# Performance work log

Hardware: AMD Instinct MI355X
Metric: run time of the kernel (lower is better)

Reference implementation:

```python
import jax, jax.numpy as jnp
import numpy as np

B, L, E = 4, 2048, 1024
H, D = 16, 64  # heads, head_dim; H*D == E


def setup_inputs() -> dict:
    key = jax.random.key(0)
    ks = jax.random.split(key, 6)
    s = 0.02
    return {
        "x": jax.random.normal(ks[0], (B, L, E), dtype=jnp.float32),
        "Wq": jax.random.normal(ks[1], (E, H * D), dtype=jnp.float32) * s,
        "Wk": jax.random.normal(ks[2], (E, H * D), dtype=jnp.float32) * s,
        "Wv": jax.random.normal(ks[3], (E, H * D), dtype=jnp.float32) * s,
        "Wo": jax.random.normal(ks[4], (H * D, E), dtype=jnp.float32) * s,
        "bo": jax.random.normal(ks[5], (E,), dtype=jnp.float32) * s,
    }


def reference(x, Wq, Wk, Wv, Wo, bo):
    b, l, e = x.shape
    q = (x @ Wq).reshape(b, l, H, D)
    k = (x @ Wk).reshape(b, l, H, D)
    v = (x @ Wv).reshape(b, l, H, D)
    # NOTE: original scales by sqrt(embed_size), not sqrt(head_dim)
    energy = jnp.einsum('nqhd,nkhd->nhqk', q, k)
    attn = jax.nn.softmax(energy / jnp.sqrt(jnp.float32(e)), axis=3)
    out = jnp.einsum('nhql,nlhd->nqhd', attn, v).reshape(b, l, H * D)
    return out @ Wo + bo
```

## Files before the change

### kernel.cpp

```cpp
#include <hip/hip_runtime.h>

#define B_ 4
#define L_ 2048
#define E_ 1024
#define H_ 16
#define D_ 64
#define CSCALE 0.045084960222629414f

typedef short s16x8 __attribute__((ext_vector_type(8)));
typedef short s16x4 __attribute__((ext_vector_type(4)));
typedef float f32x4 __attribute__((ext_vector_type(4)));

__device__ __forceinline__ unsigned short f2bf(float f) {
  union { float f; unsigned int u; } v;
  v.f = f;
  unsigned int u = v.u;
  u += 0x7fffu + ((u >> 16) & 1u);
  return (unsigned short)(u >> 16);
}

__device__ __forceinline__ unsigned short f2bf_pos(float f) {
  union { float f; unsigned int u; } v;
  v.f = f;
  return (unsigned short)((v.u + 0x8000u) >> 16);
}

__device__ __forceinline__ void async16(const void* g, void* l) {
  __builtin_amdgcn_global_load_lds(
      (__attribute__((address_space(1))) void*)(g),
      (__attribute__((address_space(3))) void*)(l), 16, 0, 0);
}

__global__ void k_prep(const float* __restrict__ x,
                       const float* __restrict__ Wq, const float* __restrict__ Wk,
                       const float* __restrict__ Wv, const float* __restrict__ Wo,
                       unsigned short* __restrict__ xb,
                       unsigned short* __restrict__ Wt, unsigned short* __restrict__ WoT) {
  __shared__ float t[32][33];
  int bid = blockIdx.x, tid = threadIdx.x;
  if (bid < 8192) {
    int i = bid * 256 + tid;
    float4 v = ((const float4*)x)[i];
    ushort4 o;
    o.x = f2bf(v.x); o.y = f2bf(v.y); o.z = f2bf(v.z); o.w = f2bf(v.w);
    ((ushort4*)xb)[i] = o;
    return;
  }
  int tt = bid - 8192;
  int wsel = tt >> 10, tile = tt & 1023;
  const float* in = (wsel == 0) ? Wq : (wsel == 1) ? Wk : (wsel == 2) ? Wv : Wo;
  unsigned short* out = (wsel == 0) ? Wt : (wsel == 1) ? Wt + (1u << 20)
                        : (wsel == 2) ? Wt + (2u << 20) : WoT;
  int bx = tile & 31, by = tile >> 5;
  int tx = tid & 31, ty = tid >> 5;
  int xcol = bx * 32 + tx;
  int y0 = by * 32;
#pragma unroll
  for (int i = 0; i < 4; ++i)
    t[ty + i * 8][tx] = in[(size_t)(y0 + ty + i * 8) * 1024 + xcol];
  __syncthreads();
  int xo = by * 32 + tx;
  int yo0 = bx * 32;
#pragma unroll
  for (int i = 0; i < 4; ++i)
    out[(size_t)(yo0 + ty + i * 8) * 1024 + xo] = f2bf(t[tx][ty + i * 8]);
}

__global__ __launch_bounds__(256) void k_gemm_qkvt(
    const unsigned short* __restrict__ xb, const unsigned short* __restrict__ Wt,
    unsigned short* __restrict__ Qb, unsigned short* __restrict__ Kb,
    unsigned short* __restrict__ Vt) {
  __shared__ __align__(16) unsigned short As[128 * 32];
  __shared__ __align__(16) unsigned short Bs[128 * 32];
  const int bid = blockIdx.x;
  const int tid = threadIdx.x;
  const int w = tid >> 6, lane = tid & 63;
  const int quad = lane >> 4, mrow = lane & 15;
  const bool isQK = bid < 1024;
  int m0, n0;
  const unsigned short *PA, *PB;
  if (isQK) {
    m0 = (bid & 63) * 128;
    n0 = (bid >> 6) * 128;
    PA = xb + (size_t)m0 * 1024;
    PB = Wt + (size_t)n0 * 1024;
  } else {
    int g = bid - 1024;
    m0 = (g & 7) * 128;
    n0 = (g >> 3) * 128;
    PA = Wt + (2u << 20) + (size_t)m0 * 1024;
    PB = xb + (size_t)n0 * 1024;
  }
  const int wr = (w >> 1) * 64, wc = (w & 1) * 64;
  const f32x4 fz = {0.f, 0.f, 0.f, 0.f};
  f32x4 acc[4][4];
#pragma unroll
  for (int a = 0; a < 4; ++a)
#pragma unroll
    for (int b = 0; b < 4; ++b) acc[a][b] = fz;

  for (int kt = 0; kt < 32; ++kt) {
    __syncthreads();
#pragma unroll
    for (int r = 0; r < 2; ++r) {
      int c = r * 256 + tid;
      int row = c >> 2, cc = c & 3;
      async16(PA + (size_t)row * 1024 + kt * 32 + cc * 8, &As[c * 8]);
    }
#pragma unroll
    for (int r = 0; r < 2; ++r) {
      int c = r * 256 + tid;
      int row = c >> 2, cc = c & 3;
      async16(PB + (size_t)row * 1024 + kt * 32 + cc * 8, &Bs[c * 8]);
    }
    __syncthreads();
    s16x8 a[4], b[4];
#pragma unroll
    for (int mt = 0; mt < 4; ++mt)
      a[mt] = *(const s16x8*)&As[(wr + mt * 16 + mrow) * 32 + quad * 8];
#pragma unroll
    for (int nt = 0; nt < 4; ++nt)
      b[nt] = *(const s16x8*)&Bs[(wc + nt * 16 + mrow) * 32 + quad * 8];
#pragma unroll
    for (int mt = 0; mt < 4; ++mt)
#pragma unroll
      for (int nt = 0; nt < 4; ++nt)
        acc[mt][nt] = __builtin_amdgcn_mfma_f32_16x16x32_bf16(a[mt], b[nt], acc[mt][nt], 0, 0, 0);
  }
  if (isQK) {
#pragma unroll
    for (int mt = 0; mt < 4; ++mt)
#pragma unroll
      for (int nt = 0; nt < 4; ++nt)
#pragma unroll
        for (int i = 0; i < 4; ++i) {
          int row = m0 + wr + mt * 16 + quad * 4 + i;
          int col = n0 + wc + nt * 16 + mrow;
          int bb = row >> 11, l = row & 2047;
          if (col < 1024) {
            int h = col >> 6, d = col & 63;
            Qb[(((size_t)(bb * 16 + h)) * 2048 + l) * 64 + d] = f2bf(acc[mt][nt][i]);
          } else {
            int c2 = col - 1024, h = c2 >> 6, d = c2 & 63;
            Kb[(((size_t)(bb * 16 + h)) * 2048 + l) * 64 + d] = f2bf(acc[mt][nt][i] * CSCALE);
          }
        }
  } else {
#pragma unroll
    for (int mt = 0; mt < 4; ++mt)
#pragma unroll
      for (int nt = 0; nt < 4; ++nt)
#pragma unroll
        for (int i = 0; i < 4; ++i) {
          int f = m0 + wr + mt * 16 + quad * 4 + i;
          int tk = n0 + wc + nt * 16 + mrow;
          int bb = tk >> 11, l = tk & 2047;
          Vt[((size_t)(bb * 1024 + f)) * 2048 + l] = f2bf(acc[mt][nt][i]);
        }
  }
}

__global__ __launch_bounds__(256, 4) void k_attn(
    const unsigned short* __restrict__ Qb, const unsigned short* __restrict__ Kb,
    const unsigned short* __restrict__ Vt, unsigned short* __restrict__ AO) {
  __shared__ __align__(16) unsigned short KVs[2][8192];
  const int tid = threadIdx.x, w = tid >> 6, lane = tid & 63;
  const int quad = lane >> 4, mrow = lane & 15;
  const int bh = blockIdx.x & 63;
  const int q0 = (blockIdx.x >> 6) * 128;
  const unsigned short* Qh = Qb + (size_t)bh * 2048 * 64;
  const unsigned short* Kh = Kb + (size_t)bh * 2048 * 64;
  const unsigned short* Vh = Vt + (size_t)bh * 64 * 2048;
  unsigned short* KVf = &KVs[0][0];

#pragma unroll
  for (int r = 0; r < 4; ++r) {
    int c = r * 256 + tid;
    int row = c >> 3, cl = c & 7;
    int gc = cl ^ (row & 7);
    async16(Qh + (size_t)(q0 + row) * 64 + gc * 8, &KVf[c * 8]);
  }
  __syncthreads();
  s16x8 qb[2][2];
#pragma unroll
  for (int nt = 0; nt < 2; ++nt)
#pragma unroll
    for (int ks = 0; ks < 2; ++ks) {
      int row = w * 32 + nt * 16 + mrow;
      qb[nt][ks] = *(const s16x8*)&KVf[row * 64 + (((ks * 4 + quad) ^ (row & 7)) << 3)];
    }
  __syncthreads();

#pragma unroll
  for (int r = 0; r < 2; ++r) {
    int c = r * 256 + tid;
    int row = c >> 3, cl = c & 7;
    int gc = cl ^ (row & 7);
    async16(Kh + (size_t)row * 64 + gc * 8, &KVs[0][c * 8]);
  }
#pragma unroll
  for (int r = 0; r < 2; ++r) {
    int c = r * 256 + tid;
    int row = c >> 3, cl = c & 7;
    int gc = cl ^ (row & 7);
    async16(Vh + (size_t)row * 2048 + gc * 8, &KVs[0][4096 + c * 8]);
  }

  const f32x4 fz = {0.f, 0.f, 0.f, 0.f};
  f32x4 o[2][4];
  float lr[2];
#pragma unroll
  for (int nt = 0; nt < 2; ++nt) {
    lr[nt] = 0.f;
#pragma unroll
    for (int dt = 0; dt < 4; ++dt) o[nt][dt] = fz;
  }

  for (int j = 0; j < 32; ++j) {
    __syncthreads();
    const unsigned short* Kt = &KVs[j & 1][0];
    const unsigned short* Vs = &KVs[j & 1][4096];

    s16x8 ak[4][2];
#pragma unroll
    for (int mt = 0; mt < 4; ++mt)
#pragma unroll
      for (int ks = 0; ks < 2; ++ks) {
        int row = mt * 16 + mrow;
        ak[mt][ks] = *(const s16x8*)&Kt[row * 64 + (((ks * 4 + quad) ^ (row & 7)) << 3)];
      }
    s16x4 vb[4][4];
#pragma unroll
    for (int dt = 0; dt < 4; ++dt)
#pragma unroll
      for (int lt = 0; lt < 4; ++lt) {
        int row = dt * 16 + mrow;
        int lbase = lt * 16 + quad * 4;
        int cg = lbase >> 3, off = lbase & 7;
        vb[dt][lt] = *(const s16x4*)&Vs[row * 64 + ((cg ^ (row & 7)) << 3) + off];
      }

    if (j + 1 < 32) {
      unsigned short* nb = &KVs[(j + 1) & 1][0];
#pragma unroll
      for (int r = 0; r < 2; ++r) {
        int c = r * 256 + tid;
        int row = c >> 3, cl = c & 7;
        int gc = cl ^ (row & 7);
        async16(Kh + (size_t)((j + 1) * 64 + row) * 64 + gc * 8, &nb[c * 8]);
      }
#pragma unroll
      for (int r = 0; r < 2; ++r) {
        int c = r * 256 + tid;
        int row = c >> 3, cl = c & 7;
        int gc = cl ^ (row & 7);
        async16(Vh + (size_t)row * 2048 + (j + 1) * 64 + gc * 8, &nb[4096 + c * 8]);
      }
    }

    f32x4 s[4][2];
#pragma unroll
    for (int mt = 0; mt < 4; ++mt)
#pragma unroll
      for (int nt = 0; nt < 2; ++nt) s[mt][nt] = fz;
#pragma unroll
    for (int ks = 0; ks < 2; ++ks)
#pragma unroll
      for (int mt = 0; mt < 4; ++mt)
#pragma unroll
        for (int nt = 0; nt < 2; ++nt)
          s[mt][nt] = __builtin_amdgcn_mfma_f32_16x16x32_bf16(ak[mt][ks], qb[nt][ks], s[mt][nt], 0, 0, 0);

    s16x4 pa[4][2];
#pragma unroll
    for (int mt = 0; mt < 4; ++mt)
#pragma unroll
      for (int nt = 0; nt < 2; ++nt) {
        float p0 = __builtin_amdgcn_exp2f(s[mt][nt][0]);
        float p1 = __builtin_amdgcn_exp2f(s[mt][nt][1]);
        float p2 = __builtin_amdgcn_exp2f(s[mt][nt][2]);
        float p3 = __builtin_amdgcn_exp2f(s[mt][nt][3]);
        lr[nt] += (p0 + p1) + (p2 + p3);
        s16x4 pk;
        pk[0] = (short)f2bf_pos(p0);
        pk[1] = (short)f2bf_pos(p1);
        pk[2] = (short)f2bf_pos(p2);
        pk[3] = (short)f2bf_pos(p3);
        pa[mt][nt] = pk;
      }

#pragma unroll
    for (int nt = 0; nt < 2; ++nt)
#pragma unroll
      for (int dt = 0; dt < 4; ++dt)
#pragma unroll
        for (int lt = 0; lt < 4; ++lt)
          o[nt][dt] = __builtin_amdgcn_mfma_f32_16x16x16bf16_1k(pa[lt][nt], vb[dt][lt], o[nt][dt], 0, 0, 0);
  }

#pragma unroll
  for (int nt = 0; nt < 2; ++nt) {
    float v = lr[nt];
    v += __shfl_xor(v, 16);
    v += __shfl_xor(v, 32);
    lr[nt] = v;
  }

  int b_ = bh >> 4, h = bh & 15;
#pragma unroll
  for (int nt = 0; nt < 2; ++nt)
#pragma unroll
    for (int i = 0; i < 4; ++i) {
      float inv = 1.f / __shfl(lr[nt], quad * 4 + i, 64);
      int qrow = q0 + w * 32 + nt * 16 + quad * 4 + i;
#pragma unroll
      for (int dt = 0; dt < 4; ++dt) {
        int d = dt * 16 + mrow;
        AO[((size_t)(b_ * 2048 + qrow)) * 1024 + h * 64 + d] = f2bf(o[nt][dt][i] * inv);
      }
    }
}

__global__ __launch_bounds__(256) void k_gemm_out(
    const unsigned short* __restrict__ Ab, const unsigned short* __restrict__ WoT,
    const float* __restrict__ bo, float* __restrict__ out) {
  __shared__ __align__(16) unsigned short As[128 * 32];
  __shared__ __align__(16) unsigned short Bs[128 * 32];
  const int tid = threadIdx.x;
  const int w = tid >> 6, lane = tid & 63;
  const int quad = lane >> 4, mrow = lane & 15;
  const int m0 = blockIdx.x * 128, n0 = blockIdx.y * 128;
  const int wr = (w >> 1) * 64, wc = (w & 1) * 64;
  const f32x4 fz = {0.f, 0.f, 0.f, 0.f};
  f32x4 acc[4][4];
#pragma unroll
  for (int a = 0; a < 4; ++a)
#pragma unroll
    for (int b = 0; b < 4; ++b) acc[a][b] = fz;

  for (int kt = 0; kt < 32; ++kt) {
    __syncthreads();
#pragma unroll
    for (int r = 0; r < 2; ++r) {
      int c = r * 256 + tid;
      int row = c >> 2, cc = c & 3;
      async16(Ab + (size_t)(m0 + row) * 1024 + kt * 32 + cc * 8, &As[c * 8]);
    }
#pragma unroll
    for (int r = 0; r < 2; ++r) {
      int c = r * 256 + tid;
      int row = c >> 2, cc = c & 3;
      async16(WoT + (size_t)(n0 + row) * 1024 + kt * 32 + cc * 8, &Bs[c * 8]);
    }
    __syncthreads();
    s16x8 a[4], b[4];
#pragma unroll
    for (int mt = 0; mt < 4; ++mt)
      a[mt] = *(const s16x8*)&As[(wr + mt * 16 + mrow) * 32 + quad * 8];
#pragma unroll
    for (int nt = 0; nt < 4; ++nt)
      b[nt] = *(const s16x8*)&Bs[(wc + nt * 16 + mrow) * 32 + quad * 8];
#pragma unroll
    for (int mt = 0; mt < 4; ++mt)
#pragma unroll
      for (int nt = 0; nt < 4; ++nt)
        acc[mt][nt] = __builtin_amdgcn_mfma_f32_16x16x32_bf16(a[mt], b[nt], acc[mt][nt], 0, 0, 0);
  }
#pragma unroll
  for (int mt = 0; mt < 4; ++mt)
#pragma unroll
    for (int nt = 0; nt < 4; ++nt)
#pragma unroll
      for (int i = 0; i < 4; ++i) {
        int row = m0 + wr + mt * 16 + quad * 4 + i;
        int col = n0 + wc + nt * 16 + mrow;
        out[(size_t)row * 1024 + col] = acc[mt][nt][i] + bo[col];
      }
}

extern "C" void kernel_launch(void* const* d_in, const int* in_sizes, int n_in,
                              void* d_out, int out_size, void* d_ws, size_t ws_size,
                              hipStream_t stream) {
  const float* x  = (const float*)d_in[0];
  const float* Wq = (const float*)d_in[1];
  const float* Wk = (const float*)d_in[2];
  const float* Wv = (const float*)d_in[3];
  const float* Wo = (const float*)d_in[4];
  const float* bo = (const float*)d_in[5];
  float* out = (float*)d_out;

  char* ws = (char*)d_ws;
  const size_t MiB = 1u << 20;
  unsigned short* xb  = (unsigned short*)(ws);
  unsigned short* Wt  = (unsigned short*)(ws + 16 * MiB);
  unsigned short* WoT = (unsigned short*)(ws + 22 * MiB);
  unsigned short* Qb  = (unsigned short*)(ws + 24 * MiB);
  unsigned short* Kb  = (unsigned short*)(ws + 40 * MiB);
  unsigned short* Vt  = (unsigned short*)(ws + 56 * MiB);
  unsigned short* AO  = xb;

  k_prep<<<12288, 256, 0, stream>>>(x, Wq, Wk, Wv, Wo, xb, Wt, WoT);
  k_gemm_qkvt<<<1536, 256, 0, stream>>>(xb, Wt, Qb, Kb, Vt);
  k_attn<<<1024, 256, 0, stream>>>(Qb, Kb, Vt, AO);
  k_gemm_out<<<dim3(64, 8), 256, 0, stream>>>(AO, WoT, bo, out);
}
```

Baseline: 286.3 us.

## Software-pipeline PV MFMA one iteration behind QK and pack bf16 with perm

Result: no change. 286.4 us (+0.0%).

```diff
diff --git a/kernel.cpp b/kernel.cpp
--- a/kernel.cpp
+++ b/kernel.cpp
@@ -19,16 +19,21 @@
   return (unsigned short)(u >> 16);
 }
 
-__device__ __forceinline__ unsigned short f2bf_pos(float f) {
-  union { float f; unsigned int u; } v;
-  v.f = f;
-  return (unsigned short)((v.u + 0x8000u) >> 16);
-}
-
 __device__ __forceinline__ void async16(const void* g, void* l) {
   __builtin_amdgcn_global_load_lds(
       (__attribute__((address_space(1))) void*)(g),
       (__attribute__((address_space(3))) void*)(l), 16, 0, 0);
+}
+
+__device__ __forceinline__ s16x4 pack4bf(float p0, float p1, float p2, float p3) {
+  union { float f; unsigned int u; } a0, a1, a2, a3;
+  a0.f = p0; a1.f = p1; a2.f = p2; a3.f = p3;
+  unsigned int r0 = a0.u + 0x8000u, r1 = a1.u + 0x8000u;
+  unsigned int r2 = a2.u + 0x8000u, r3 = a3.u + 0x8000u;
+  union { s16x4 v; unsigned int u[2]; } out;
+  out.u[0] = __builtin_amdgcn_perm(r1, r0, 0x07060302);
+  out.u[1] = __builtin_amdgcn_perm(r3, r2, 0x07060302);
+  return out.v;
 }
 
 __global__ void k_prep(const float* __restrict__ x,
@@ -160,7 +165,7 @@
   }
 }
 
-__global__ __launch_bounds__(256, 4) void k_attn(
+__global__ __launch_bounds__(256, 2) void k_attn(
     const unsigned short* __restrict__ Qb, const unsigned short* __restrict__ Kb,
     const unsigned short* __restrict__ Vt, unsigned short* __restrict__ AO) {
   __shared__ __align__(16) unsigned short KVs[2][8192];
@@ -215,6 +220,8 @@
 #pragma unroll
     for (int dt = 0; dt < 4; ++dt) o[nt][dt] = fz;
   }
+  s16x4 vbp[4][4];
+  s16x4 pap[4][2];
 
   for (int j = 0; j < 32; ++j) {
     __syncthreads();
@@ -271,7 +278,16 @@
         for (int nt = 0; nt < 2; ++nt)
           s[mt][nt] = __builtin_amdgcn_mfma_f32_16x16x32_bf16(ak[mt][ks], qb[nt][ks], s[mt][nt], 0, 0, 0);
 
-    s16x4 pa[4][2];
+    if (j) {
+#pragma unroll
+      for (int nt = 0; nt < 2; ++nt)
+#pragma unroll
+        for (int dt = 0; dt < 4; ++dt)
+#pragma unroll
+          for (int lt = 0; lt < 4; ++lt)
+            o[nt][dt] = __builtin_amdgcn_mfma_f32_16x16x16bf16_1k(pap[lt][nt], vbp[dt][lt], o[nt][dt], 0, 0, 0);
+    }
+
 #pragma unroll
     for (int mt = 0; mt < 4; ++mt)
 #pragma unroll
@@ -281,22 +297,20 @@
         float p2 = __builtin_amdgcn_exp2f(s[mt][nt][2]);
         float p3 = __builtin_amdgcn_exp2f(s[mt][nt][3]);
         lr[nt] += (p0 + p1) + (p2 + p3);
-        s16x4 pk;
-        pk[0] = (short)f2bf_pos(p0);
-        pk[1] = (short)f2bf_pos(p1);
-        pk[2] = (short)f2bf_pos(p2);
-        pk[3] = (short)f2bf_pos(p3);
-        pa[mt][nt] = pk;
-      }
-
-#pragma unroll
-    for (int nt = 0; nt < 2; ++nt)
-#pragma unroll
-      for (int dt = 0; dt < 4; ++dt)
-#pragma unroll
-        for (int lt = 0; lt < 4; ++lt)
-          o[nt][dt] = __builtin_amdgcn_mfma_f32_16x16x16bf16_1k(pa[lt][nt], vb[dt][lt], o[nt][dt], 0, 0, 0);
-  }
+        pap[mt][nt] = pack4bf(p0, p1, p2, p3);
+      }
+#pragma unroll
+    for (int dt = 0; dt < 4; ++dt)
+#pragma unroll
+      for (int lt = 0; lt < 4; ++lt) vbp[dt][lt] = vb[dt][lt];
+  }
+#pragma unroll
+  for (int nt = 0; nt < 2; ++nt)
+#pragma unroll
+    for (int dt = 0; dt < 4; ++dt)
+#pragma unroll
+      for (int lt = 0; lt < 4; ++lt)
+        o[nt][dt] = __builtin_amdgcn_mfma_f32_16x16x16bf16_1k(pap[lt][nt], vbp[dt][lt], o[nt][dt], 0, 0, 0);
 
 #pragma unroll
   for (int nt = 0; nt < 2; ++nt) {
```
